# Performance work log

Hardware: AMD Instinct MI355X
Metric: run time of the kernel (lower is better)

Reference implementation:

```python
import jax, jax.numpy as jnp
import numpy as np

S = 17          # number of segment ids (0 = background, skipped)
MIN_H = 100.0   # HomographySmoothLoss.min_segment_pixels
MIN_V = 50.0    # ObjectVarianceLoss.min_segment_pixels
SUPPRESS = 0.1  # BoundaryAwareSmoothLoss.boundary_suppress


def _maxpool3(x):
    # torch F.max_pool2d(k=3, stride=1, pad=1) pads with -inf
    return jax.lax.reduce_window(x, -jnp.inf, jax.lax.max,
                                 (1, 1, 3, 3), (1, 1, 1, 1),
                                 ((0, 0), (0, 0), (1, 1), (1, 1)))


def _boundary_map(masks):
    lab = masks.astype(jnp.float32)[:, None]  # (B,1,H,W)
    dil = _maxpool3(lab)
    ero = -_maxpool3(-lab)
    return (dil != ero).astype(jnp.float32)


def _nearest(x, Ho, Wo):
    # torch F.interpolate(mode='nearest'): src = floor(dst * in/out)
    H, W = x.shape[-2], x.shape[-1]
    yi = (jnp.arange(Ho) * H) // Ho
    xi = (jnp.arange(Wo) * W) // Wo
    return x[..., yi, :][..., :, xi]


def _conv3(x, k):
    return jax.lax.conv_general_dilated(x, k, (1, 1), ((1, 1), (1, 1)),
                                        dimension_numbers=('NCHW', 'OIHW', 'NCHW'))


def _segment_losses(flow, masks):
    # Vectorized replacement of per-(batch,segment) python loops:
    # accumulate per-segment moments with segment_sum, then batched 3x3
    # normal-equation solves (equivalent to torch.lstsq affine fit).
    B, _, H, W = flow.shape
    NS = B * S
    xs = jnp.broadcast_to(jnp.arange(W, dtype=jnp.float32)[None, None, :], (B, H, W)).reshape(-1)
    ys = jnp.broadcast_to(jnp.arange(H, dtype=jnp.float32)[None, :, None], (B, H, W)).reshape(-1)
    u = flow[:, 0].reshape(-1)
    v = flow[:, 1].reshape(-1)
    seg = masks.reshape(-1)
    bidx = jnp.repeat(jnp.arange(B, dtype=jnp.int32), H * W)
    idx = bidx * S + seg                                  # global segment id
    ones = jnp.ones_like(xs)
    feats = jnp.stack([ones, xs, ys, xs * xs, xs * ys, ys * ys,
                       u, v, u * u, v * v, xs * u, ys * u, xs * v, ys * v], axis=1)
    sums = jax.ops.segment_sum(feats, idx, num_segments=NS)  # (NS,14)
    (n, Sx, Sy, Sxx, Sxy, Syy, Su, Sv, Suu, Svv,
     Sxu, Syu, Sxv, Syv) = [sums[:, i] for i in range(14)]
    segids = jnp.tile(jnp.arange(S), B)

    # ---- homography loss: per-segment affine least-squares fit ----
    valid_h = (segids != 0) & (n >= MIN_H)
    ATA = jnp.stack([jnp.stack([Sxx, Sxy, Sx], -1),
                     jnp.stack([Sxy, Syy, Sy], -1),
                     jnp.stack([Sx, Sy, n], -1)], axis=1)   # (NS,3,3)
    eye3 = jnp.eye(3, dtype=flow.dtype)
    ATA = jnp.where(valid_h[:, None, None], ATA, eye3)      # keep solve nonsingular
    ATb = jnp.stack([jnp.stack([Sxu, Sxv], -1),
                     jnp.stack([Syu, Syv], -1),
                     jnp.stack([Su, Sv], -1)], axis=1)      # (NS,3,2)
    ATb = jnp.where(valid_h[:, None, None], ATb, 0.0)
    params = jnp.linalg.solve(ATA, ATb)                     # (NS,3,2): [a,b,c] for u and v
    p = params[idx]                                         # (BHW,3,2) gather per pixel
    pred_u = xs * p[:, 0, 0] + ys * p[:, 1, 0] + p[:, 2, 0]
    pred_v = xs * p[:, 0, 1] + ys * p[:, 1, 1] + p[:, 2, 1]
    res = jnp.sqrt((u - pred_u) ** 2 + (v - pred_v) ** 2)
    res_mean = jax.ops.segment_sum(res, idx, num_segments=NS) / jnp.maximum(n, 1.0)
    nh = jnp.maximum(jnp.sum(valid_h), 1)
    homog = jnp.sum(res_mean * valid_h) / nh

    # ---- object variance loss (unbiased var, matches torch .var()) ----
    valid_v = (segids != 0) & (n >= MIN_V)
    nsafe = jnp.maximum(n, 2.0)
    var_u = (Suu - Su * Su / nsafe) / (nsafe - 1.0)
    var_v = (Svv - Sv * Sv / nsafe) / (nsafe - 1.0)
    nv = jnp.maximum(jnp.sum(valid_v), 1)
    ovar = jnp.sum((var_u + var_v) * valid_v) / nv
    return homog, ovar


def setup_inputs():
    key = jax.random.key(0)
    k1, k2, k3 = jax.random.split(key, 3)
    B, H, W = 8, 512, 1024
    flow = jax.random.normal(k1, (B, 2, H, W), jnp.float32)
    masks = jax.random.randint(k2, (B, H, W), 0, S).astype(jnp.int32)
    images = jax.random.uniform(k3, (B, 3, H, W), jnp.float32)
    return {"flow": flow, "masks": masks, "images": images}


def reference(flow, masks, images):
    boundary = _boundary_map(masks)                         # (B,1,H,W)
    homog, ovar = _segment_losses(flow, masks)

    # ---- boundary sharpness (sobel on flow magnitude) ----
    sobel_x = jnp.array([[-1., 0., 1.], [-2., 0., 2.], [-1., 0., 1.]], jnp.float32).reshape(1, 1, 3, 3)
    sobel_y = jnp.array([[-1., -2., -1.], [0., 0., 0.], [1., 2., 1.]], jnp.float32).reshape(1, 1, 3, 3)
    flow_mag = jnp.sqrt(jnp.sum(flow ** 2, axis=1, keepdims=True))
    fg = jnp.abs(_conv3(flow_mag, sobel_x)) + jnp.abs(_conv3(flow_mag, sobel_y))
    fg = fg / (jnp.max(fg) + 1e-6)
    bn = boundary / (jnp.max(boundary) + 1e-6)
    sharp = jnp.mean(bn * (1.0 - fg))

    # ---- boundary-aware edge-weighted smoothness ----
    flow_dx = flow[:, :, :, 1:] - flow[:, :, :, :-1]
    flow_dy = flow[:, :, 1:, :] - flow[:, :, :-1, :]
    g = jnp.mean(images, axis=1, keepdims=True)
    wx = jnp.exp(-jnp.abs(g[:, :, :, 1:] - g[:, :, :, :-1]) * 10.0)
    wy = jnp.exp(-jnp.abs(g[:, :, 1:, :] - g[:, :, :-1, :]) * 10.0)
    bx = _nearest(boundary, wx.shape[2], wx.shape[3])
    by = _nearest(boundary, wy.shape[2], wy.shape[3])
    wx = wx * (1.0 - (1.0 - SUPPRESS) * bx)
    wy = wy * (1.0 - (1.0 - SUPPRESS) * by)
    smooth = jnp.mean(jnp.abs(flow_dx) * wx) + jnp.mean(jnp.abs(flow_dy) * wy)

    # weights all 1.0; order: homography, boundary_sharpness, object_variance, boundary_smooth
    return jnp.stack([homog, sharp, ovar, smooth])
```

## Files before the change

### kernel.cpp

```cpp
#include <hip/hip_runtime.h>
#include <math.h>

#define BB 8
#define HH 512
#define WW 1024
#define HW (HH * WW)
#define NPIX (BB * HW)
#define NSEG 16
#define SUPPRESS 0.1f


__device__ __forceinline__ float wave_sum(float t) {
    #pragma unroll
    for (int off = 32; off > 0; off >>= 1) t += __shfl_down(t, off);
    return t;
}

#define REP8(M) M(0) M(1) M(2) M(3) M(4) M(5) M(6) M(7)

__global__ __launch_bounds__(64) void moments_kernel(
    const float* __restrict__ flow,
    const int*   __restrict__ masks,
    double* __restrict__ moments4)
{
    __shared__ float bins[9984];

    const int lane = threadIdx.x;
    const int bid  = blockIdx.x;
    const int colg = bid & 15;
    const int rowg = (bid >> 4) & 7;
    const int b    = bid >> 7;
    const int par  = bid & 3;

    const int c0 = colg * 64;
    const int r0 = rowg * 64;

    const float* fu = flow + (long long)b * (2LL * HW);
    const float* fv = fu + HW;
    const int*   mk = masks + (long long)b * HW;
    const int*   mrow = mk + r0 * WW + c0 + lane;
    const float* urow = fu + r0 * WW + c0 + lane;
    const float* vrow = fv + r0 * WW + c0 + lane;

    #pragma unroll
    for (int i = 0; i < 39; ++i)
        *(float4*)&bins[i * 256 + lane * 4] = make_float4(0.f, 0.f, 0.f, 0.f);

    int   m0 = mrow[0];
    float u0 = urow[0], v0 = vrow[0];
    int   m1 = mrow[WW];
    float u1 = urow[WW], v1 = vrow[WW];

    #pragma unroll 1
    for (int r = 0; r < 64; r += 2) {
        const int o2 = ((r + 2) & 63) * WW;
        const int o3 = ((r + 3) & 63) * WW;
        const int   m2 = mrow[o2];
        const float u2 = urow[o2], v2 = vrow[o2];
        const int   m3 = mrow[o3];
        const float u3 = urow[o3], v3 = vrow[o3];

        {
            const float y = (float)(r0 + r);
            float* bp = &bins[m0 * 576 + lane];
            float b0 = bp[0],   b1 = bp[64],  b2 = bp[128];
            float b3 = bp[192], b4 = bp[256], b5 = bp[320];
            float b6 = bp[384], b7 = bp[448], b8 = bp[512];
            b0 += 1.f;
            b1 += y;
            b2 = fmaf(y, y, b2);
            b3 += u0;
            b4 += v0;
            b5 = fmaf(u0, u0, b5);
            b6 = fmaf(v0, v0, b6);
            b7 = fmaf(y, u0, b7);
            b8 = fmaf(y, v0, b8);
            bp[0] = b0;   bp[64] = b1;  bp[128] = b2;
            bp[192] = b3; bp[256] = b4; bp[320] = b5;
            bp[384] = b6; bp[448] = b7; bp[512] = b8;
        }
        {
            const float y = (float)(r0 + r + 1);
            float* bp = &bins[m1 * 576 + lane];
            float b0 = bp[0],   b1 = bp[64],  b2 = bp[128];
            float b3 = bp[192], b4 = bp[256], b5 = bp[320];
            float b6 = bp[384], b7 = bp[448], b8 = bp[512];
            b0 += 1.f;
            b1 += y;
            b2 = fmaf(y, y, b2);
            b3 += u1;
            b4 += v1;
            b5 = fmaf(u1, u1, b5);
            b6 = fmaf(v1, v1, b6);
            b7 = fmaf(y, u1, b7);
            b8 = fmaf(y, v1, b8);
            bp[0] = b0;   bp[64] = b1;  bp[128] = b2;
            bp[192] = b3; bp[256] = b4; bp[320] = b5;
            bp[384] = b6; bp[448] = b7; bp[512] = b8;
        }
        m0 = m2; u0 = u2; v0 = v2;
        m1 = m3; u1 = u3; v1 = v3;
    }

    const unsigned long long SRC = 0x84736543210100ULL;
    const unsigned long long PW  = 0x01010000012010ULL;
    double* cell = moments4 + par * 1792 + b * 224;
    #pragma unroll 1
    for (int rp = 0; rp < 4; ++rp) {
        const int p   = rp * 64 + lane;
        const int act = (p < 224);
        const int pc  = act ? p : 0;
        const int segm = pc / 14;
        const int feat = pc - segm * 14;
        const int srcb = (int)((SRC >> (4 * feat)) & 15);
        const int pw   = (int)((PW  >> (4 * feat)) & 15);
        const float* bp = &bins[(segm + 1) * 576 + srcb * 64];
        float acc = 0.f;
        #pragma unroll 8
        for (int l0 = 0; l0 < 64; ++l0) {
            const int l = (l0 + lane) & 63;
            const float xv = (float)(c0 + l);
            const float w = (pw == 0) ? 1.f : ((pw == 1) ? xv : xv * xv);
            acc = fmaf(bp[l], w, acc);
        }
        if (act) atomicAdd(&cell[segm * 14 + feat], (double)acc);
    }
}

__global__ __launch_bounds__(256) void stencil_kernel(
    const float* __restrict__ flow,
    const int*   __restrict__ masks,
    const float* __restrict__ images,
    double* __restrict__ scal64,
    unsigned* __restrict__ maxfg64)
{
    __shared__ float    smX[4][260], smW[4][260];
    __shared__ unsigned mX[4][260],  mW[4][260];
    __shared__ float    gX[2][260];
    __shared__ float    ue[2][260],  ve[2][260];
    __shared__ float    wred[4][5];

    const int tid = threadIdx.x;
    const int lane = tid & 63;
    const long long base = (long long)blockIdx.x * 2048;
    const int b  = (int)(base >> 19);
    const int h0 = (int)((base & (HW - 1)) >> 10);

    const float* fu = flow + (long long)b * (2LL * HW);
    const float* fv = fu + HW;
    const int*   mk = masks + (long long)b * HW;
    const float* i0 = images + (long long)b * (3LL * HW);
    const float* i1 = i0 + HW;
    const float* i2 = i1 + HW;

    const int c4 = tid * 4;
    float4 m4a[4];
    unsigned mbp[4];
    float4 ur[3], vr[3];
    float4 gr[3];

    #pragma unroll
    for (int r = 0; r < 4; ++r) {
        const int grow = h0 - 1 + r;
        const int mr = grow < 0 ? 0 : (grow > HH - 1 ? HH - 1 : grow);
        const int4 mv = *(const int4*)&mk[mr * WW + c4];
        mbp[r] = (unsigned)(mv.x & 255) | ((unsigned)(mv.y & 255) << 8) |
                 ((unsigned)(mv.z & 255) << 16) | ((unsigned)(mv.w & 255) << 24);

        float4 u4 = make_float4(0.f, 0.f, 0.f, 0.f);
        float4 v4 = make_float4(0.f, 0.f, 0.f, 0.f);
        if (grow >= 0 && grow <= HH - 1) {
            u4 = *(const float4*)&fu[grow * WW + c4];
            v4 = *(const float4*)&fv[grow * WW + c4];
        }
        float4 m4;
        m4.x = sqrtf(u4.x * u4.x + v4.x * v4.x);
        m4.y = sqrtf(u4.y * u4.y + v4.y * v4.y);
        m4.z = sqrtf(u4.z * u4.z + v4.z * v4.z);
        m4.w = sqrtf(u4.w * u4.w + v4.w * v4.w);
        m4a[r] = m4;
        smX[r][tid] = m4.x;
        smW[r][tid + 1] = m4.w;
        mX[r][tid] = (unsigned)(mv.x & 255);
        mW[r][tid + 1] = (unsigned)(mv.w & 255);
        if (tid == 0)   { smW[r][0] = 0.f;   mW[r][0] = (unsigned)(mv.x & 255); }
        if (tid == 255) { smX[r][256] = 0.f; mX[r][256] = (unsigned)(mv.w & 255); }
        if (r >= 1) { ur[r - 1] = u4; vr[r - 1] = v4; }
    }
    #pragma unroll
    for (int r = 0; r < 3; ++r) {
        const int grow = h0 + r;
        float4 g4 = make_float4(0.f, 0.f, 0.f, 0.f);
        if (grow <= HH - 1) {
            const float4 a  = *(const float4*)&i0[grow * WW + c4];
            const float4 bq = *(const float4*)&i1[grow * WW + c4];
            const float4 c  = *(const float4*)&i2[grow * WW + c4];
            g4.x = (a.x + bq.x + c.x) * (1.f / 3.f);
            g4.y = (a.y + bq.y + c.y) * (1.f / 3.f);
            g4.z = (a.z + bq.z + c.z) * (1.f / 3.f);
            g4.w = (a.w + bq.w + c.w) * (1.f / 3.f);
        }
        gr[r] = g4;
        if (r < 2) gX[r][tid] = g4.x;
    }
    ue[0][tid] = ur[0].x; ve[0][tid] = vr[0].x;
    ue[1][tid] = ur[1].x; ve[1][tid] = vr[1].x;
    __syncthreads();

    float a_dx = 0.f, a_dy = 0.f, a_sb = 0.f, a_sbf = 0.f, mfg = 0.f;

    #pragma unroll
    for (int lr = 0; lr < 2; ++lr) {
        const int h = h0 + lr;
        float a[3][6];
        unsigned long long kw[3];
        #pragma unroll
        for (int r = 0; r < 3; ++r) {
            const int rr = lr + r;
            const float4 own = m4a[rr];
            a[r][0] = smW[rr][tid];
            a[r][1] = own.x; a[r][2] = own.y; a[r][3] = own.z; a[r][4] = own.w;
            a[r][5] = smX[rr][tid + 1];
            kw[r] = (unsigned long long)mW[rr][tid]
                  | ((unsigned long long)mbp[rr] << 8)
                  | ((unsigned long long)mX[rr][tid + 1] << 40);
        }
        const float4 gc = gr[lr];
        const float4 gd4 = gr[lr + 1];
        const float gval[5] = {gc.x, gc.y, gc.z, gc.w, gX[lr][tid + 1]};
        const float gd[4]  = {gd4.x, gd4.y, gd4.z, gd4.w};
        const float4 uc4 = ur[lr],  vc4 = vr[lr];
        const float4 ud4 = ur[lr + 1], vd4 = vr[lr + 1];
        const float uc[5] = {uc4.x, uc4.y, uc4.z, uc4.w, ue[lr][tid + 1]};
        const float vc[5] = {vc4.x, vc4.y, vc4.z, vc4.w, ve[lr][tid + 1]};
        const float ud[4] = {ud4.x, ud4.y, ud4.z, ud4.w};
        const float vd[4] = {vd4.x, vd4.y, vd4.z, vd4.w};

        #pragma unroll
        for (int j = 0; j < 4; ++j) {
            const int w = c4 + j;
            const unsigned cseg = (unsigned)((kw[1] >> (8 * (j + 1))) & 255);
            int bnd = (((kw[0] >> (8 * j)) & 255) != cseg)
                    | (((kw[0] >> (8 * (j + 1))) & 255) != cseg)
                    | (((kw[0] >> (8 * (j + 2))) & 255) != cseg)
                    | (((kw[1] >> (8 * j)) & 255) != cseg)
                    | (((kw[1] >> (8 * (j + 2))) & 255) != cseg)
                    | (((kw[2] >> (8 * j)) & 255) != cseg)
                    | (((kw[2] >> (8 * (j + 1))) & 255) != cseg)
                    | (((kw[2] >> (8 * (j + 2))) & 255) != cseg);

            const float fgx = (a[0][j + 2] - a[0][j]) + 2.f * (a[1][j + 2] - a[1][j]) +
                              (a[2][j + 2] - a[2][j]);
            const float fgy = (a[2][j] + 2.f * a[2][j + 1] + a[2][j + 2]) -
                              (a[0][j] + 2.f * a[0][j + 1] + a[0][j + 2]);
            const float fgraw = fabsf(fgx) + fabsf(fgy);
            mfg = fmaxf(mfg, fgraw);
            if (bnd) { a_sb += 1.f; a_sbf += fgraw; }

            const float u = uc[j], v = vc[j], g0 = gval[j];
            if (w < WW - 1) {
                const float wgt = expf(-fabsf(gval[j + 1] - g0) * 10.f) * (bnd ? SUPPRESS : 1.f);
                a_dx += (fabsf(uc[j + 1] - u) + fabsf(vc[j + 1] - v)) * wgt;
            }
            if (h < HH - 1) {
                const float wgt = expf(-fabsf(gd[j] - g0) * 10.f) * (bnd ? SUPPRESS : 1.f);
                a_dy += (fabsf(ud[j] - u) + fabsf(vd[j] - v)) * wgt;
            }
        }
    }

    for (int off = 32; off > 0; off >>= 1) {
        a_dx += __shfl_down(a_dx, off);
        a_dy += __shfl_down(a_dy, off);
        a_sb += __shfl_down(a_sb, off);
        a_sbf += __shfl_down(a_sbf, off);
        mfg = fmaxf(mfg, __shfl_down(mfg, off));
    }
    if (lane == 0) {
        const int wv = tid >> 6;
        wred[wv][0] = a_dx; wred[wv][1] = a_dy; wred[wv][2] = a_sb;
        wred[wv][3] = a_sbf; wred[wv][4] = mfg;
    }
    __syncthreads();
    if (tid == 0) {
        float dx = 0.f, dy = 0.f, sb = 0.f, sbf = 0.f, mf = 0.f;
        for (int i = 0; i < 4; ++i) {
            dx += wred[i][0]; dy += wred[i][1]; sb += wred[i][2];
            sbf += wred[i][3]; mf = fmaxf(mf, wred[i][4]);
        }
        const int sl = blockIdx.x & 63;
        atomicAdd(&scal64[sl * 4 + 0], (double)dx);
        atomicAdd(&scal64[sl * 4 + 1], (double)dy);
        atomicAdd(&scal64[sl * 4 + 2], (double)sb);
        atomicAdd(&scal64[sl * 4 + 3], (double)sbf);
        atomicMax(&maxfg64[sl], __float_as_uint(mf));
    }
}

__global__ __launch_bounds__(128) void solve_kernel(
    const double* __restrict__ moments4,
    float* __restrict__ params,
    int* __restrict__ valid,
    float* __restrict__ out)
{
    const int i = threadIdx.x;
    double m[14];
    #pragma unroll
    for (int k = 0; k < 14; ++k) {
        double s = 0.0;
        #pragma unroll
        for (int par = 0; par < 4; ++par) s += moments4[par * 1792 + i * 14 + k];
        m[k] = s;
    }
    const double n = m[0];
    const int vh = (n >= 100.0) ? 1 : 0;
    float p[6] = {0.f, 0.f, 0.f, 0.f, 0.f, 0.f};
    if (vh) {
        double A[3][3] = {{m[3], m[4], m[1]},
                          {m[4], m[5], m[2]},
                          {m[1], m[2], n}};
        double Bm[3][2] = {{m[10], m[12]},
                           {m[11], m[13]},
                           {m[6],  m[7]}};
        for (int k = 0; k < 3; ++k) {
            int piv = k; double mx = fabs(A[k][k]);
            for (int r = k + 1; r < 3; ++r) {
                double a = fabs(A[r][k]);
                if (a > mx) { mx = a; piv = r; }
            }
            if (piv != k) {
                for (int c = 0; c < 3; ++c) { double t = A[k][c]; A[k][c] = A[piv][c]; A[piv][c] = t; }
                for (int c = 0; c < 2; ++c) { double t = Bm[k][c]; Bm[k][c] = Bm[piv][c]; Bm[piv][c] = t; }
            }
            const double inv = 1.0 / A[k][k];
            for (int r = k + 1; r < 3; ++r) {
                const double f = A[r][k] * inv;
                for (int c = k; c < 3; ++c) A[r][c] -= f * A[k][c];
                Bm[r][0] -= f * Bm[k][0];
                Bm[r][1] -= f * Bm[k][1];
            }
        }
        double X[3][2];
        for (int c = 0; c < 2; ++c) {
            X[2][c] = Bm[2][c] / A[2][2];
            X[1][c] = (Bm[1][c] - A[1][2] * X[2][c]) / A[1][1];
            X[0][c] = (Bm[0][c] - A[0][1] * X[1][c] - A[0][2] * X[2][c]) / A[0][0];
        }
        p[0] = (float)X[0][0]; p[1] = (float)X[1][0]; p[2] = (float)X[2][0];
        p[3] = (float)X[0][1]; p[4] = (float)X[1][1]; p[5] = (float)X[2][1];
    }
    valid[i] = vh;
    for (int c = 0; c < 6; ++c) params[i * 6 + c] = p[c];

    const int vv = (n >= 50.0) ? 1 : 0;
    double var = 0.0;
    if (vv) {
        const double ns = (n > 2.0) ? n : 2.0;
        const double var_u = (m[8] - m[6] * m[6] / ns) / (ns - 1.0);
        const double var_v = (m[9] - m[7] * m[7] / ns) / (ns - 1.0);
        var = var_u + var_v;
    }
    __shared__ double svar[128];
    __shared__ int scnt[128];
    svar[i] = var; scnt[i] = vv;
    __syncthreads();
    for (int s = 64; s > 0; s >>= 1) {
        if (i < s) { svar[i] += svar[i + s]; scnt[i] += scnt[i + s]; }
        __syncthreads();
    }
    if (i == 0) out[2] = (float)(svar[0] / (double)(scnt[0] > 1 ? scnt[0] : 1));
}

__global__ __launch_bounds__(256) void pass2_kernel(
    const float* __restrict__ flow,
    const int*   __restrict__ masks,
    const float* __restrict__ params,
    double* __restrict__ res4)
{
    __shared__ float sp[17 * 6];

    const long long base = (long long)blockIdx.x * 4096;
    const int b      = (int)(base >> 19);
    const int hwbase = (int)(base & (HW - 1));
    const int tid    = threadIdx.x;
    const int lane   = tid & 63;

    if (tid < 6) sp[tid] = 0.f;
    if (tid < 96) sp[6 + tid] = params[b * 96 + tid];
    __syncthreads();

    const float* fu = flow + (long long)b * (2LL * HW);
    const float* fv = fu + HW;
    const int*   mk = masks + (long long)b * HW;

#define DECLR(i) float r_##i = 0.f;
    REP8(DECLR)
#define DECLR2(i) float q_##i = 0.f;
    REP8(DECLR2)

    #pragma unroll
    for (int it = 0; it < 4; ++it) {
        const int i4 = hwbase + it * 1024 + tid * 4;
        const int4   m4 = *(const int4*)&mk[i4];
        const float4 u4 = *(const float4*)&fu[i4];
        const float4 v4 = *(const float4*)&fv[i4];
        const int segs[4] = {m4.x, m4.y, m4.z, m4.w};
        const float us[4] = {u4.x, u4.y, u4.z, u4.w};
        const float vs[4] = {v4.x, v4.y, v4.z, v4.w};
        #pragma unroll
        for (int j = 0; j < 4; ++j) {
            const int seg = segs[j];
            const float* pf = &sp[seg * 6];
            const int hw = i4 + j;
            const float x = (float)(hw & 1023), y = (float)((hw & (HW - 1)) >> 10);
            const float du = us[j] - (x * pf[0] + y * pf[1] + pf[2]);
            const float dv = vs[j] - (x * pf[3] + y * pf[4] + pf[5]);
            const float r = sqrtf(du * du + dv * dv);
            const int sr = seg - 1;
#define STEPR(i) r_##i += (sr == i) ? r : 0.f;
            REP8(STEPR)
#define STEPR2(i) q_##i += (sr == 8 + i) ? r : 0.f;
            REP8(STEPR2)
        }
    }

    const int par = blockIdx.x & 3;
    double* rb = &res4[par * 128 + b * 16];
#define FINR(i) { const float s = wave_sum(r_##i); \
    if (lane == 0) atomicAdd(rb + i, (double)s); }
    REP8(FINR)
#define FINR2(i) { const float s = wave_sum(q_##i); \
    if (lane == 0) atomicAdd(rb + 8 + i, (double)s); }
    REP8(FINR2)
}

__global__ __launch_bounds__(128) void final_kernel(
    const double* __restrict__ moments4,
    const double* __restrict__ res4,
    const int*    __restrict__ valid,
    const double* __restrict__ scal64,
    const unsigned* __restrict__ maxfg64,
    float* __restrict__ out)
{
    const int i = threadIdx.x;
    double n = 0.0, rs = 0.0;
    #pragma unroll
    for (int par = 0; par < 4; ++par) {
        n  += moments4[par * 1792 + i * 14];
        rs += res4[par * 128 + i];
    }
    const int vh = valid[i];
    const double rm = vh ? rs / (n > 1.0 ? n : 1.0) : 0.0;
    __shared__ double sr[128];
    __shared__ int sc[128];
    sr[i] = rm; sc[i] = vh;
    __syncthreads();
    for (int s = 64; s > 0; s >>= 1) {
        if (i < s) { sr[i] += sr[i + s]; sc[i] += sc[i + s]; }
        __syncthreads();
    }
    if (i == 0) {
        out[0] = (float)(sr[0] / (double)(sc[0] > 1 ? sc[0] : 1));
        double dx = 0.0, dy = 0.0, sb = 0.0, sbf = 0.0;
        float mf = 0.f;
        for (int k = 0; k < 64; ++k) {
            dx += scal64[k * 4 + 0]; dy += scal64[k * 4 + 1];
            sb += scal64[k * 4 + 2]; sbf += scal64[k * 4 + 3];
            mf = fmaxf(mf, __uint_as_float(maxfg64[k]));
        }
        const double maxfg = (double)mf;
        const double maxb = (sb > 0.0) ? 1.0 : 0.0;
        out[1] = (float)((sb - sbf / (maxfg + 1e-6)) / (maxb + 1e-6) / (double)NPIX);
        const double smooth = dx / (double)(2LL * BB * HH * (WW - 1)) +
                              dy / (double)(2LL * BB * (HH - 1) * WW);
        out[3] = (float)smooth;
    }
}

extern "C" void kernel_launch(void* const* d_in, const int* in_sizes, int n_in,
                              void* d_out, int out_size, void* d_ws, size_t ws_size,
                              hipStream_t stream)
{
    const float* flow   = (const float*)d_in[0];
    const int*   masks  = (const int*)d_in[1];
    const float* images = (const float*)d_in[2];
    float* out = (float*)d_out;

    char* ws = (char*)d_ws;
    double*   moments4 = (double*)(ws);
    double*   res4     = (double*)(ws + 57344);
    double*   scal64   = (double*)(ws + 61440);
    unsigned* maxfg64  = (unsigned*)(ws + 63488);
    float*    params   = (float*)(ws + 63744);
    int*      valid    = (int*)(ws + 66816);

    hipMemsetAsync(d_ws, 0, 67584, stream);

    moments_kernel<<<dim3(1024), dim3(64), 0, stream>>>(flow, masks, moments4);
    stencil_kernel<<<dim3(NPIX / 2048), dim3(256), 0, stream>>>(
        flow, masks, images, scal64, maxfg64);
    solve_kernel<<<dim3(1), dim3(128), 0, stream>>>(moments4, params, valid, out);
    pass2_kernel<<<dim3(NPIX / 4096), dim3(256), 0, stream>>>(
        flow, masks, params, res4);
    final_kernel<<<dim3(1), dim3(128), 0, stream>>>(
        moments4, res4, valid, scal64, maxfg64, out);
}
```

Measured before the change: 110.5 us.

## Split per-segment moment accumulation across four waves per block

The moments kernel moves from one 64-thread wave per tile to four waves. Each wave owns a disjoint subset of the nine shared-memory bins, so the LDS read-modify-write chain per pixel is spread across waves instead of being serialised in one. The final reduction maps one thread per output cell, and barriers are added around zeroing and accumulation. In exchange, every wave now reloads the same flow and mask data, and the branch on wave id adds some control overhead.

```diff
diff --git a/kernel.cpp b/kernel.cpp
--- a/kernel.cpp
+++ b/kernel.cpp
@@ -18,14 +18,16 @@
 
 #define REP8(M) M(0) M(1) M(2) M(3) M(4) M(5) M(6) M(7)
 
-__global__ __launch_bounds__(64) void moments_kernel(
+__global__ __launch_bounds__(256) void moments_kernel(
     const float* __restrict__ flow,
     const int*   __restrict__ masks,
     double* __restrict__ moments4)
 {
     __shared__ float bins[9984];
 
-    const int lane = threadIdx.x;
+    const int tid  = threadIdx.x;
+    const int lane = tid & 63;
+    const int wid  = tid >> 6;
     const int bid  = blockIdx.x;
     const int colg = bid & 15;
     const int rowg = (bid >> 4) & 7;
@@ -42,14 +44,35 @@
     const float* urow = fu + r0 * WW + c0 + lane;
     const float* vrow = fv + r0 * WW + c0 + lane;
 
-    #pragma unroll
-    for (int i = 0; i < 39; ++i)
-        *(float4*)&bins[i * 256 + lane * 4] = make_float4(0.f, 0.f, 0.f, 0.f);
+    for (int i = tid; i < 2496; i += 256)
+        *(float4*)&bins[i * 4] = make_float4(0.f, 0.f, 0.f, 0.f);
+    __syncthreads();
 
     int   m0 = mrow[0];
     float u0 = urow[0], v0 = vrow[0];
     int   m1 = mrow[WW];
     float u1 = urow[WW], v1 = vrow[WW];
+
+#define MPROC(RR, MM, UU, VV) { \
+    const float y = (float)(r0 + (RR)); \
+    float* bp = &bins[(MM) * 576 + lane]; \
+    if (wid == 0) { \
+        float b0 = bp[0], b1 = bp[64], b2 = bp[128]; \
+        b0 += 1.f; b1 += y; b2 = fmaf(y, y, b2); \
+        bp[0] = b0; bp[64] = b1; bp[128] = b2; \
+    } else if (wid == 1) { \
+        float b3 = bp[192], b5 = bp[320]; \
+        b3 += (UU); b5 = fmaf((UU), (UU), b5); \
+        bp[192] = b3; bp[320] = b5; \
+    } else if (wid == 2) { \
+        float b4 = bp[256], b6 = bp[384]; \
+        b4 += (VV); b6 = fmaf((VV), (VV), b6); \
+        bp[256] = b4; bp[384] = b6; \
+    } else { \
+        float b7 = bp[448], b8 = bp[512]; \
+        b7 = fmaf(y, (UU), b7); b8 = fmaf(y, (VV), b8); \
+        bp[448] = b7; bp[512] = b8; \
+    } }
 
     #pragma unroll 1
     for (int r = 0; r < 64; r += 2) {
@@ -60,54 +83,19 @@
         const int   m3 = mrow[o3];
         const float u3 = urow[o3], v3 = vrow[o3];
 
-        {
-            const float y = (float)(r0 + r);
-            float* bp = &bins[m0 * 576 + lane];
-            float b0 = bp[0],   b1 = bp[64],  b2 = bp[128];
-            float b3 = bp[192], b4 = bp[256], b5 = bp[320];
-            float b6 = bp[384], b7 = bp[448], b8 = bp[512];
-            b0 += 1.f;
-            b1 += y;
-            b2 = fmaf(y, y, b2);
-            b3 += u0;
-            b4 += v0;
-            b5 = fmaf(u0, u0, b5);
-            b6 = fmaf(v0, v0, b6);
-            b7 = fmaf(y, u0, b7);
-            b8 = fmaf(y, v0, b8);
-            bp[0] = b0;   bp[64] = b1;  bp[128] = b2;
-            bp[192] = b3; bp[256] = b4; bp[320] = b5;
-            bp[384] = b6; bp[448] = b7; bp[512] = b8;
-        }
-        {
-            const float y = (float)(r0 + r + 1);
-            float* bp = &bins[m1 * 576 + lane];
-            float b0 = bp[0],   b1 = bp[64],  b2 = bp[128];
-            float b3 = bp[192], b4 = bp[256], b5 = bp[320];
-            float b6 = bp[384], b7 = bp[448], b8 = bp[512];
-            b0 += 1.f;
-            b1 += y;
-            b2 = fmaf(y, y, b2);
-            b3 += u1;
-            b4 += v1;
-            b5 = fmaf(u1, u1, b5);
-            b6 = fmaf(v1, v1, b6);
-            b7 = fmaf(y, u1, b7);
-            b8 = fmaf(y, v1, b8);
-            bp[0] = b0;   bp[64] = b1;  bp[128] = b2;
-            bp[192] = b3; bp[256] = b4; bp[320] = b5;
-            bp[384] = b6; bp[448] = b7; bp[512] = b8;
-        }
+        MPROC(r, m0, u0, v0)
+        MPROC(r + 1, m1, u1, v1)
+
         m0 = m2; u0 = u2; v0 = v2;
         m1 = m3; u1 = u3; v1 = v3;
     }
+    __syncthreads();
 
     const unsigned long long SRC = 0x84736543210100ULL;
     const unsigned long long PW  = 0x01010000012010ULL;
     double* cell = moments4 + par * 1792 + b * 224;
-    #pragma unroll 1
-    for (int rp = 0; rp < 4; ++rp) {
-        const int p   = rp * 64 + lane;
+    {
+        const int p   = tid;
         const int act = (p < 224);
         const int pc  = act ? p : 0;
         const int segm = pc / 14;
@@ -496,7 +484,7 @@
 
     hipMemsetAsync(d_ws, 0, 67584, stream);
 
-    moments_kernel<<<dim3(1024), dim3(64), 0, stream>>>(flow, masks, moments4);
+    moments_kernel<<<dim3(1024), dim3(256), 0, stream>>>(flow, masks, moments4);
     stencil_kernel<<<dim3(NPIX / 2048), dim3(256), 0, stream>>>(
         flow, masks, images, scal64, maxfg64);
     solve_kernel<<<dim3(1), dim3(128), 0, stream>>>(moments4, params, valid, out);
```

Result: no change. 108.8 us (-1.5%).
